# Performance work log

Hardware: AMD Instinct MI355X
Metric: run time of the kernel (lower is better)

The kernel has to match this reference:

```python
import jax, jax.numpy as jnp
import numpy as np

BS, T, SIDE, H, Z, NSPK = 2048, 34, 30, 128, 16, 1024


def _lrelu(x):
    # nn.LeakyReLU(True) -> negative_slope=1.0, i.e. identity (faithful to source)
    return x


def _gru_cell(x, h, wih, whh, bih, bhh):
    # PyTorch GRU cell, gate order (r, z, n)
    gi = x @ wih.T + bih
    gh = h @ whh.T + bhh
    ir, iz, inn = jnp.split(gi, 3, axis=-1)
    hr, hz, hn = jnp.split(gh, 3, axis=-1)
    r = jax.nn.sigmoid(ir + hr)
    z = jax.nn.sigmoid(iz + hz)
    n = jnp.tanh(inn + r * hn)
    return (1.0 - z) * n + z * h


def setup_inputs() -> dict:
    key = jax.random.key(0)
    ks = iter(jax.random.split(key, 64))
    rn = lambda shape, s=0.05: jax.random.normal(next(ks), shape, jnp.float32) * s
    inp = {}
    inp["pre_seq"] = jax.random.normal(next(ks), (BS, T, 28), jnp.float32)
    inp["beats"] = jax.random.normal(next(ks), (BS, 2, T * SIDE), jnp.float32)
    inp["in_text"] = jnp.zeros((BS, T), jnp.int32)   # unused by forward
    inp["in_audio"] = jnp.zeros((BS, 1), jnp.float32)  # unused by forward
    inp["vid_indices"] = jax.random.randint(next(ks), (BS,), 0, NSPK)
    inp["eps"] = jax.random.normal(next(ks), (BS, Z), jnp.float32)  # reparameterize noise
    # speaker embedding net
    inp["spk_table"] = rn((NSPK, Z))
    inp["spk_lin_w"] = rn((Z, Z)); inp["spk_lin_b"] = jnp.zeros((Z,))
    inp["mu_w"] = rn((Z, Z)); inp["mu_b"] = jnp.zeros((Z,))
    inp["lv_w"] = rn((Z, Z)); inp["lv_b"] = jnp.zeros((Z,))
    # per-step MLPs
    inp["squ_w"] = rn((H, 3 * SIDE)); inp["squ_b"] = jnp.zeros((H,))
    inp["oenv_w"] = rn((H, 3 * SIDE)); inp["oenv_b"] = jnp.zeros((H,))
    inp["pose_w"] = rn((16, 28)); inp["pose_b"] = jnp.zeros((16,))
    inp["out_w"] = rn((H, H + 16)); inp["out_b"] = jnp.zeros((H,))
    inp["bo_w1"] = rn((64, H)); inp["bo_b1"] = jnp.zeros((64,))
    inp["bo_w2"] = rn((27, 64)); inp["bo_b2"] = jnp.zeros((27,))
    # GRU: 4 layers, bidirectional, hidden 128; layer0 input 144, layers1-3 input 256
    inp["w_ih_l0"] = rn((2, 3 * H, H + 16)); inp["w_hh_l0"] = rn((2, 3 * H, H))
    inp["b_ih_l0"] = jnp.zeros((2, 3 * H)); inp["b_hh_l0"] = jnp.zeros((2, 3 * H))
    inp["w_ih"] = rn((3, 2, 3 * H, 2 * H)); inp["w_hh"] = rn((3, 2, 3 * H, H))
    inp["b_ih"] = jnp.zeros((3, 2, 3 * H)); inp["b_hh"] = jnp.zeros((3, 2, 3 * H))
    return inp


def reference(pre_seq, beats, in_text, in_audio, vid_indices, eps,
              spk_table, spk_lin_w, spk_lin_b, mu_w, mu_b, lv_w, lv_b,
              squ_w, squ_b, oenv_w, oenv_b, pose_w, pose_b,
              out_w, out_b, bo_w1, bo_b1, bo_w2, bo_b2,
              w_ih_l0, w_hh_l0, b_ih_l0, b_hh_l0, w_ih, w_hh, b_ih, b_hh):
    bs = beats.shape[0]
    # speaker latent
    zc0 = spk_table[vid_indices] @ spk_lin_w.T + spk_lin_b
    z_mu = zc0 @ mu_w.T + mu_b
    z_logvar = zc0 @ lv_w.T + lv_b
    z_context = z_mu + eps * jnp.exp(0.5 * z_logvar)  # reparameterize

    # sub_beats windows: pad side_size zeros on each end, window=90, stride=30
    padded = jnp.pad(beats, ((0, 0), (0, 0), (SIDE, SIDE)))
    widx = SIDE * jnp.arange(T)[:, None] + jnp.arange(3 * SIDE)[None, :]
    win = padded[:, :, widx]  # (bs, 2, T, 90)

    # batch the tiny per-step MLPs across all 34 steps at once
    squ = _lrelu(jnp.einsum('bts,os->bto', win[:, 0], squ_w) + squ_b)
    oenv = _lrelu(jnp.einsum('bts,os->bto', win[:, 1], oenv_w) + oenv_b)
    sum_out = squ + oenv                                   # (bs, T, 128)
    pose = _lrelu(jnp.einsum('bts,os->bto', pre_seq, pose_w) + pose_b)  # (bs, T, 16)
    xs = jnp.concatenate([pose, sum_out], axis=-1).transpose(1, 0, 2)   # (T, bs, 144)

    def step(h, x):
        # h: (8, bs, H) = [l0_fwd, l0_bwd, l1_fwd, ...]; seq_len==1 per step
        hs = []
        for l in range(4):
            if l == 0:
                wi, wh, bi, bh = w_ih_l0, w_hh_l0, b_ih_l0, b_hh_l0
            else:
                wi, wh, bi, bh = w_ih[l - 1], w_hh[l - 1], b_ih[l - 1], b_hh[l - 1]
            hf = _gru_cell(x, h[2 * l], wi[0], wh[0], bi[0], bh[0])
            hb = _gru_cell(x, h[2 * l + 1], wi[1], wh[1], bi[1], bh[1])
            hs += [hf, hb]
            x = jnp.concatenate([hf, hb], axis=-1)
        # output = fwd half + bwd half of top layer
        return jnp.stack(hs), hs[-2] + hs[-1]

    h0 = jnp.zeros((8, bs, H), xs.dtype)  # decoder_hidden = None -> zeros
    _, outs = jax.lax.scan(step, h0, xs)  # (T, bs, H)

    zb = jnp.broadcast_to(z_context, (T,) + z_context.shape)  # (T, bs, 16)
    feat = _lrelu(jnp.concatenate([outs, zb], axis=-1) @ out_w.T + out_b)  # (T, bs, 128)
    beat = _lrelu(feat @ bo_w1.T + bo_b1) @ bo_w2.T + bo_b2               # (T, bs, 27)
    return beat.transpose(1, 0, 2), z_context, z_mu, z_logvar
```

## Files before the change

kernel.cpp:

```cpp
#include <hip/hip_runtime.h>
#include <hip/hip_bf16.h>
#include <stdint.h>

typedef __attribute__((ext_vector_type(8))) short bfrag;
typedef __attribute__((ext_vector_type(4))) float f32x4;

__device__ __forceinline__ unsigned short f2bf(float f){
  union { float f; unsigned u; } v; v.f = f;
  unsigned r = v.u + 0x7FFFu + ((v.u >> 16) & 1u);
  return (unsigned short)(r >> 16);
}
__device__ __forceinline__ f32x4 mfma16(bfrag a, bfrag b, f32x4 c){
  return __builtin_amdgcn_mfma_f32_16x16x32_bf16(a, b, c, 0, 0, 0);
}
__device__ __forceinline__ bfrag cvt8(const float* s){
  bfrag r;
  #pragma unroll
  for (int j = 0; j < 8; ++j) r[j] = (short)f2bf(s[j]);
  return r;
}

__global__ void k_pad(const float* __restrict__ beats, unsigned short* __restrict__ pad,
                      int NG){
  int g = blockIdx.x * 256 + threadIdx.x;
  if (g >= NG) return;
  int i8 = (g % 135) * 8;
  long rc = g / 135;
  const float* src = beats + rc * 1020;
  union { unsigned short u[8]; bfrag s; } o;
  #pragma unroll
  for (int j = 0; j < 8; ++j){
    int i = i8 + j;
    float v = (i >= 30 && i < 1050) ? src[i - 30] : 0.f;
    o.u[j] = f2bf(v);
  }
  *(bfrag*)(pad + rc * 1080 + i8) = o.s;
}

__global__ void k_prep(const float* __restrict__ squ_w, const float* __restrict__ oenv_w,
                       const float* __restrict__ pose_w, const float* __restrict__ out_w,
                       const float* __restrict__ bo_w1, const float* __restrict__ bo_w2,
                       unsigned short* __restrict__ B2w, unsigned short* __restrict__ posewp,
                       unsigned short* __restrict__ B1, unsigned short* __restrict__ bow1p,
                       unsigned short* __restrict__ bow2p){
  int i = blockIdx.x * 256 + threadIdx.x;
  if (i < 24576){
    int o = i / 192, k = i - o * 192;
    float v = 0.f;
    if (k < 90) v = squ_w[o * 90 + k];
    else if (k >= 96 && k < 186) v = oenv_w[o * 90 + (k - 96)];
    B2w[i] = f2bf(v);
    return;
  }
  i -= 24576;
  if (i < 512){
    int o = i / 32, k = i - o * 32;
    posewp[i] = f2bf(k < 28 ? pose_w[o * 28 + k] : 0.f);
    return;
  }
  i -= 512;
  if (i < 36864){
    int o = i / 288, k = i - o * 288;
    float v = 0.f;
    if (k < 128) v = out_w[o * 144 + k];
    else if (k < 256) v = out_w[o * 144 + (k - 128)];
    else if (k < 272) v = out_w[o * 144 + 128 + (k - 256)];
    B1[i] = f2bf(v);
    return;
  }
  i -= 36864;
  if (i < 8192){ bow1p[i] = f2bf(bo_w1[i]); return; }
  i -= 8192;
  if (i < 2048){
    int o = i / 64, k = i - o * 64;
    bow2p[i] = f2bf(o < 27 ? bo_w2[o * 64 + k] : 0.f);
  }
}

__global__ void k_z(const int* __restrict__ vid, const float* __restrict__ eps,
                    const float* __restrict__ spk_table, const float* __restrict__ slw,
                    const float* __restrict__ slb, const float* __restrict__ muw,
                    const float* __restrict__ mub, const float* __restrict__ lvw,
                    const float* __restrict__ lvb,
                    float* __restrict__ outp, unsigned short* __restrict__ zws){
  int b = blockIdx.x * 256 + threadIdx.x;
  if (b >= 2048) return;
  const float* tr = spk_table + (long)vid[b] * 16;
  float t[16], zc0[16];
  #pragma unroll
  for (int k = 0; k < 16; ++k) t[k] = tr[k];
  #pragma unroll
  for (int j = 0; j < 16; ++j){
    float a = slb[j];
    #pragma unroll
    for (int k = 0; k < 16; ++k) a += t[k] * slw[j * 16 + k];
    zc0[j] = a;
  }
  const long ZC = 1880064, ZMU = 1912832, ZLV = 1945600;
  #pragma unroll
  for (int j = 0; j < 16; ++j){
    float mu = mub[j], lv = lvb[j];
    #pragma unroll
    for (int k = 0; k < 16; ++k){ mu += zc0[k] * muw[j * 16 + k]; lv += zc0[k] * lvw[j * 16 + k]; }
    float zc = mu + eps[b * 16 + j] * __expf(0.5f * lv);
    outp[ZMU + b * 16 + j] = mu;
    outp[ZLV + b * 16 + j] = lv;
    outp[ZC + b * 16 + j] = zc;
    zws[b * 16 + j] = f2bf(zc);
  }
}

__global__ __launch_bounds__(256) void k_x0(
    const unsigned short* __restrict__ pad, const float* __restrict__ pre_seq,
    const unsigned short* __restrict__ B2w, const unsigned short* __restrict__ posewp,
    const float* __restrict__ squ_b, const float* __restrict__ oenv_b,
    const float* __restrict__ pose_b, unsigned short* __restrict__ xbuf0){
  int bid = blockIdx.x;
  int t = bid % 34, bt = bid / 34;
  int w = threadIdx.x >> 6, lane = threadIdx.x & 63;
  int q = lane >> 4, l15 = lane & 15;
  int row = bt * 64 + w * 16 + l15;
  bfrag a[6];
  {
    const unsigned short* p0 = pad + ((long)row * 2) * 1080 + 30 * t;
    #pragma unroll
    for (int kt = 0; kt < 6; ++kt){
      int k = kt * 32 + q * 8;
      const unsigned short* src = (k < 96) ? (p0 + k) : (p0 + 1080 + (k - 96));
      const unsigned int* pu = (const unsigned int*)src;
      union { unsigned int u[4]; bfrag s; } v;
      v.u[0] = pu[0]; v.u[1] = pu[1]; v.u[2] = pu[2]; v.u[3] = pu[3];
      a[kt] = v.s;
    }
  }
  f32x4 acc[8];
  #pragma unroll
  for (int nt = 0; nt < 8; ++nt) acc[nt] = (f32x4){0.f, 0.f, 0.f, 0.f};
  #pragma unroll
  for (int kt = 0; kt < 6; ++kt)
    #pragma unroll
    for (int nt = 0; nt < 8; ++nt){
      bfrag bf = *(const bfrag*)(B2w + ((nt * 16 + l15) * 192 + kt * 32 + q * 8));
      acc[nt] = mfma16(a[kt], bf, acc[nt]);
    }
  f32x4 accp = (f32x4){0.f, 0.f, 0.f, 0.f};
  {
    float av[8];
    const float* ps = pre_seq + ((long)row * 34 + t) * 28;
    if (q < 3){
      #pragma unroll
      for (int j = 0; j < 8; ++j) av[j] = ps[q * 8 + j];
    } else {
      #pragma unroll
      for (int j = 0; j < 4; ++j){ av[j] = ps[24 + j]; av[4 + j] = 0.f; }
    }
    bfrag ap = cvt8(av);
    bfrag bp = *(const bfrag*)(posewp + (l15 * 32 + q * 8));
    accp = mfma16(ap, bp, accp);
  }
  float pb = pose_b[l15];
  int rowc = bt * 64 + w * 16 + q * 4;
  #pragma unroll
  for (int r = 0; r < 4; ++r){
    long base = ((long)(rowc + r) * 34 + t) * 160;
    xbuf0[base + l15] = f2bf(accp[r] + pb);
    xbuf0[base + 144 + l15] = 0;
  }
  #pragma unroll
  for (int nt = 0; nt < 8; ++nt){
    int c = nt * 16 + l15;
    float sb = squ_b[c] + oenv_b[c];
    #pragma unroll
    for (int r = 0; r < 4; ++r){
      long base = ((long)(rowc + r) * 34 + t) * 160;
      xbuf0[base + 16 + c] = f2bf(acc[nt][r] + sb);
    }
  }
}

template<int KIT, int KI>
__global__ __launch_bounds__(512, 2) void k_gru(
    const unsigned short* __restrict__ xin, unsigned short* __restrict__ xout,
    const float* __restrict__ wih, const float* __restrict__ whh,
    const float* __restrict__ bih, const float* __restrict__ bhh, int WK){
  __shared__ unsigned short x_lds[3][16 * (KI + 8)];
  __shared__ unsigned short h_lds[2][16 * 136];
  int d = blockIdx.x & 1, bt = blockIdx.x >> 1;
  int tid = threadIdx.x;
  int w = tid >> 6, lane = tid & 63, q = lane >> 4, l15 = lane & 15;
  const float* wihd = wih + (long)d * 384 * WK;
  const float* whhd = whh + (long)d * 384 * 128;
  int col = w * 16 + l15;
  float bi0 = bih[d * 384 + col], bi1 = bih[d * 384 + 128 + col], bi2 = bih[d * 384 + 256 + col];
  float bh0 = bhh[d * 384 + col], bh1 = bhh[d * 384 + 128 + col], bh2 = bhh[d * 384 + 256 + col];
  bfrag bgi[3][KIT];
  #pragma unroll
  for (int g = 0; g < 3; ++g)
    #pragma unroll
    for (int kt = 0; kt < KIT; ++kt){
      int k = kt * 32 + q * 8;
      if (k < WK){
        float tmp[8];
        const float* s = wihd + (long)(g * 128 + col) * WK + k;
        #pragma unroll
        for (int j = 0; j < 8; ++j) tmp[j] = s[j];
        bgi[g][kt] = cvt8(tmp);
      } else {
        bgi[g][kt] = (bfrag){0, 0, 0, 0, 0, 0, 0, 0};
      }
    }
  bfrag bwh[3][4];
  #pragma unroll
  for (int g = 0; g < 3; ++g)
    #pragma unroll
    for (int kt = 0; kt < 4; ++kt){
      float tmp[8];
      const float* s = whhd + (long)(g * 128 + col) * 128 + kt * 32 + q * 8;
      #pragma unroll
      for (int j = 0; j < 8; ++j) tmp[j] = s[j];
      bwh[g][kt] = cvt8(tmp);
    }
  const int NV = KI / 8;
  int xrow = tid / NV, xv = tid - xrow * NV;
  bool xact = (tid < 16 * NV);
  const unsigned short* xin_row = xin + ((long)(bt * 16 + (xact ? xrow : 0))) * 34 * KI;
  if (xact){
    *(bfrag*)(&x_lds[0][xrow * (KI + 8) + xv * 8]) = *(const bfrag*)(xin_row + xv * 8);
    *(bfrag*)(&x_lds[1][xrow * (KI + 8) + xv * 8]) = *(const bfrag*)(xin_row + (long)KI + xv * 8);
  }
  for (int i = tid; i < 16 * 136; i += 512) h_lds[0][i] = 0;
  __syncthreads();

  f32x4 gc0 = {0,0,0,0}, gc1 = {0,0,0,0}, gc2 = {0,0,0,0};
  #pragma unroll
  for (int kt = 0; kt < KIT; ++kt){
    bfrag xa = *(const bfrag*)(&x_lds[0][l15 * (KI + 8) + kt * 32 + q * 8]);
    gc0 = mfma16(xa, bgi[0][kt], gc0);
    gc1 = mfma16(xa, bgi[1][kt], gc1);
    gc2 = mfma16(xa, bgi[2][kt], gc2);
  }
  bfrag xpf = (bfrag){0, 0, 0, 0, 0, 0, 0, 0};
  if (xact) xpf = *(const bfrag*)(xin_row + 2L * KI + xv * 8);

  f32x4 h_old = {0,0,0,0};
  unsigned short hbf[4] = {0, 0, 0, 0};
  int rowc = bt * 16 + q * 4;
  int p = 0;
  int s1 = 1, s2 = 2;
  for (int t = 0; t < 34; ++t){
    if (t > 0){
      #pragma unroll
      for (int r = 0; r < 4; ++r)
        xout[((long)(rowc + r) * 34 + (t - 1)) * 256 + d * 128 + col] = hbf[r];
    }
    f32x4 gh0 = {0,0,0,0}, gh1 = {0,0,0,0}, gh2 = {0,0,0,0};
    #pragma unroll
    for (int kt = 0; kt < 4; ++kt){
      bfrag ha = *(const bfrag*)(&h_lds[p][l15 * 136 + kt * 32 + q * 8]);
      gh0 = mfma16(ha, bwh[0][kt], gh0);
      gh1 = mfma16(ha, bwh[1][kt], gh1);
      gh2 = mfma16(ha, bwh[2][kt], gh2);
    }
    f32x4 h_new;
    #pragma unroll
    for (int r = 0; r < 4; ++r){
      float ir = gc0[r] + bi0, iz = gc1[r] + bi1, inn = gc2[r] + bi2;
      float hr = gh0[r] + bh0, hz = gh1[r] + bh1, hn = gh2[r] + bh2;
      float rg = 1.f / (1.f + __expf(-(ir + hr)));
      float zg = 1.f / (1.f + __expf(-(iz + hz)));
      float pre = inn + rg * hn;
      float ax = fabsf(pre);
      float th = 1.f - 2.f / (__expf(2.f * ax) + 1.f);
      th = (pre < 0.f) ? -th : th;
      float hv = (1.f - zg) * th + zg * h_old[r];
      h_new[r] = hv;
      hbf[r] = f2bf(hv);
    }
    h_old = h_new;
    #pragma unroll
    for (int r = 0; r < 4; ++r)
      h_lds[1 - p][(q * 4 + r) * 136 + col] = hbf[r];
    if (t + 1 < 34){
      f32x4 gn0 = {0,0,0,0}, gn1 = {0,0,0,0}, gn2 = {0,0,0,0};
      #pragma unroll
      for (int kt = 0; kt < KIT; ++kt){
        bfrag xa = *(const bfrag*)(&x_lds[s1][l15 * (KI + 8) + kt * 32 + q * 8]);
        gn0 = mfma16(xa, bgi[0][kt], gn0);
        gn1 = mfma16(xa, bgi[1][kt], gn1);
        gn2 = mfma16(xa, bgi[2][kt], gn2);
      }
      gc0 = gn0; gc1 = gn1; gc2 = gn2;
    }
    if (xact && t + 2 < 34){
      *(bfrag*)(&x_lds[s2][xrow * (KI + 8) + xv * 8]) = xpf;
      if (t + 3 < 34) xpf = *(const bfrag*)(xin_row + (long)(t + 3) * KI + xv * 8);
    }
    s1 = (s1 == 2) ? 0 : s1 + 1;
    s2 = (s2 == 2) ? 0 : s2 + 1;
    p ^= 1;
    __syncthreads();
  }
  #pragma unroll
  for (int r = 0; r < 4; ++r)
    xout[((long)(rowc + r) * 34 + 33) * 256 + d * 128 + col] = hbf[r];
}

__global__ __launch_bounds__(512) void k_head(
    const unsigned short* __restrict__ xb, const unsigned short* __restrict__ zloc,
    const unsigned short* __restrict__ B1p, const unsigned short* __restrict__ bow1p,
    const unsigned short* __restrict__ bow2p,
    const float* __restrict__ out_b, const float* __restrict__ bo_b1,
    const float* __restrict__ bo_b2, float* __restrict__ outp){
  __shared__ unsigned short B1_lds[128 * 296];
  __shared__ unsigned short feat_lds[128 * 136];
  __shared__ unsigned short bt1_lds[128 * 72];
  int tid = threadIdx.x, w = tid >> 6, lane = tid & 63, q = lane >> 4, l15 = lane & 15;
  long rbase = (long)blockIdx.x * 128;
  for (int v = tid; v < 128 * 36; v += 512){
    int n = v / 36, kc = (v - n * 36) * 8;
    *(bfrag*)(&B1_lds[n * 296 + kc]) = *(const bfrag*)(B1p + n * 288 + kc);
  }
  __syncthreads();
  int rloc = w * 16 + l15;
  long rt = rbase + rloc;
  int bidx = (int)(rt / 34);
  bfrag a1[9];
  #pragma unroll
  for (int kt = 0; kt < 8; ++kt)
    a1[kt] = *(const bfrag*)(xb + rt * 256 + kt * 32 + q * 8);
  if (q < 2) a1[8] = *(const bfrag*)(zloc + (long)bidx * 16 + q * 8);
  else       a1[8] = (bfrag){0, 0, 0, 0, 0, 0, 0, 0};
  f32x4 acc[8];
  #pragma unroll
  for (int nt = 0; nt < 8; ++nt) acc[nt] = (f32x4){0.f, 0.f, 0.f, 0.f};
  #pragma unroll
  for (int kt = 0; kt < 9; ++kt)
    #pragma unroll
    for (int nt = 0; nt < 8; ++nt){
      bfrag b = *(const bfrag*)(&B1_lds[(nt * 16 + l15) * 296 + kt * 32 + q * 8]);
      acc[nt] = mfma16(a1[kt], b, acc[nt]);
    }
  #pragma unroll
  for (int nt = 0; nt < 8; ++nt){
    float bb = out_b[nt * 16 + l15];
    #pragma unroll
    for (int r = 0; r < 4; ++r)
      feat_lds[(w * 16 + q * 4 + r) * 136 + nt * 16 + l15] = f2bf(acc[nt][r] + bb);
  }
  __syncthreads();
  bfrag a2[4];
  #pragma unroll
  for (int kt = 0; kt < 4; ++kt)
    a2[kt] = *(const bfrag*)(&feat_lds[rloc * 136 + kt * 32 + q * 8]);
  f32x4 acc2[4];
  #pragma unroll
  for (int nt = 0; nt < 4; ++nt) acc2[nt] = (f32x4){0.f, 0.f, 0.f, 0.f};
  #pragma unroll
  for (int kt = 0; kt < 4; ++kt)
    #pragma unroll
    for (int nt = 0; nt < 4; ++nt){
      bfrag b = *(const bfrag*)(bow1p + ((nt * 16 + l15) * 128 + kt * 32 + q * 8));
      acc2[nt] = mfma16(a2[kt], b, acc2[nt]);
    }
  #pragma unroll
  for (int nt = 0; nt < 4; ++nt){
    float bb = bo_b1[nt * 16 + l15];
    #pragma unroll
    for (int r = 0; r < 4; ++r)
      bt1_lds[(w * 16 + q * 4 + r) * 72 + nt * 16 + l15] = f2bf(acc2[nt][r] + bb);
  }
  __syncthreads();
  bfrag a3[2];
  #pragma unroll
  for (int kt = 0; kt < 2; ++kt)
    a3[kt] = *(const bfrag*)(&bt1_lds[rloc * 72 + kt * 32 + q * 8]);
  f32x4 acc3[2];
  #pragma unroll
  for (int nt = 0; nt < 2; ++nt) acc3[nt] = (f32x4){0.f, 0.f, 0.f, 0.f};
  #pragma unroll
  for (int kt = 0; kt < 2; ++kt)
    #pragma unroll
    for (int nt = 0; nt < 2; ++nt){
      bfrag b = *(const bfrag*)(bow2p + ((nt * 16 + l15) * 64 + kt * 32 + q * 8));
      acc3[nt] = mfma16(a3[kt], b, acc3[nt]);
    }
  #pragma unroll
  for (int nt = 0; nt < 2; ++nt){
    int n = nt * 16 + l15;
    if (n < 27){
      float bb = bo_b2[n];
      #pragma unroll
      for (int r = 0; r < 4; ++r){
        long rowg = rbase + w * 16 + q * 4 + r;
        outp[rowg * 27 + n] = acc3[nt][r] + bb;
      }
    }
  }
}

extern "C" void kernel_launch(void* const* d_in, const int* in_sizes, int n_in,
                              void* d_out, int out_size, void* d_ws, size_t ws_size,
                              hipStream_t stream){
  (void)in_sizes; (void)n_in; (void)out_size;
  const float* pre_seq = (const float*)d_in[0];
  const float* beats   = (const float*)d_in[1];
  const int*   vid     = (const int*)d_in[4];
  const float* eps     = (const float*)d_in[5];
  const float* spk_table = (const float*)d_in[6];
  const float* slw = (const float*)d_in[7];
  const float* slb = (const float*)d_in[8];
  const float* muw = (const float*)d_in[9];
  const float* mub = (const float*)d_in[10];
  const float* lvw = (const float*)d_in[11];
  const float* lvb = (const float*)d_in[12];
  const float* squ_w = (const float*)d_in[13];
  const float* squ_b = (const float*)d_in[14];
  const float* oenv_w = (const float*)d_in[15];
  const float* oenv_b = (const float*)d_in[16];
  const float* pose_w = (const float*)d_in[17];
  const float* pose_b = (const float*)d_in[18];
  const float* out_w = (const float*)d_in[19];
  const float* out_b = (const float*)d_in[20];
  const float* bo_w1 = (const float*)d_in[21];
  const float* bo_b1 = (const float*)d_in[22];
  const float* bo_w2 = (const float*)d_in[23];
  const float* bo_b2 = (const float*)d_in[24];
  const float* w_ih_l0 = (const float*)d_in[25];
  const float* w_hh_l0 = (const float*)d_in[26];
  const float* b_ih_l0 = (const float*)d_in[27];
  const float* b_hh_l0 = (const float*)d_in[28];
  const float* w_ih = (const float*)d_in[29];
  const float* w_hh = (const float*)d_in[30];
  const float* b_ih = (const float*)d_in[31];
  const float* b_hh = (const float*)d_in[32];
  float* outp = (float*)d_out;
  unsigned short* ws = (unsigned short*)d_ws;

  const long o_z     = 0;
  const long o_B2w   = 32768;
  const long o_posew = o_B2w + 24576;
  const long o_B1    = o_posew + 512;
  const long o_bw1   = o_B1 + 36864;
  const long o_bw2   = o_bw1 + 8192;
  const long o_chunk = o_bw2 + 2048;

  int Bc;
  {
    const size_t margin = 1u << 20;
    size_t need2048 = (size_t)(o_chunk + 2048L * 25008) * 2 + margin;
    size_t need512  = (size_t)(o_chunk + 512L  * 25008) * 2 + margin;
    if      (ws_size >= need2048) Bc = 2048;
    else if (ws_size >= need512)  Bc = 512;
    else                          Bc = 128;
  }
  const int C = 2048 / Bc;
  const long o_pad = o_chunk;
  const long o_x0  = o_pad + (long)Bc * 2160;
  const long o_A   = o_x0  + (long)Bc * 5440;
  const long o_B   = o_A   + (long)Bc * 8704;

  k_prep<<<282, 256, 0, stream>>>(squ_w, oenv_w, pose_w, out_w, bo_w1, bo_w2,
                                  ws + o_B2w, ws + o_posew, ws + o_B1, ws + o_bw1, ws + o_bw2);
  k_z<<<8, 256, 0, stream>>>(vid, eps, spk_table, slw, slb, muw, mub, lvw, lvb, outp, ws + o_z);

  for (int c = 0; c < C; ++c){
    long b0 = (long)c * Bc;
    int NG = Bc * 270;
    k_pad<<<NG / 256, 256, 0, stream>>>(beats + b0 * 2040, ws + o_pad, NG);
    k_x0<<<34 * (Bc / 64), 256, 0, stream>>>(ws + o_pad, pre_seq + b0 * 952,
                                             ws + o_B2w, ws + o_posew,
                                             squ_b, oenv_b, pose_b, ws + o_x0);
    k_gru<5, 160><<<Bc / 8, 512, 0, stream>>>(ws + o_x0, ws + o_A,
                                              w_ih_l0, w_hh_l0, b_ih_l0, b_hh_l0, 144);
    k_gru<8, 256><<<Bc / 8, 512, 0, stream>>>(ws + o_A, ws + o_B,
                                              w_ih, w_hh, b_ih, b_hh, 256);
    k_gru<8, 256><<<Bc / 8, 512, 0, stream>>>(ws + o_B, ws + o_A,
                                              w_ih + 1L * 2 * 384 * 256, w_hh + 1L * 2 * 384 * 128,
                                              b_ih + 2 * 384, b_hh + 2 * 384, 256);
    k_gru<8, 256><<<Bc / 8, 512, 0, stream>>>(ws + o_A, ws + o_B,
                                              w_ih + 2L * 2 * 384 * 256, w_hh + 2L * 2 * 384 * 128,
                                              b_ih + 4 * 384, b_hh + 4 * 384, 256);
    k_head<<<Bc * 34 / 128, 512, 0, stream>>>(ws + o_B, ws + o_z,
                                              ws + o_B1, ws + o_bw1, ws + o_bw2,
                                              out_b, bo_b1, bo_b2, outp + b0 * 918);
  }
}
```

Before: 499.1 us.

## Split GRU layers into input-projection and recurrence kernels with 8-row recurrent blocks

Each fused GRU layer kernel becomes two kernels. The first computes the input-gate projections for all timesteps and stores them in bf16 in a workspace buffer. The second runs only the hidden-state recurrence, with each block handling 8 batch rows and 256 threads, so the serial chain is shorter per step and twice as many blocks run in parallel. The cost is extra global memory traffic for the gate buffer, gate inputs rounded to bf16, and half the MFMA rows wasted in the recurrence, since only 8 of the 16 are used.

```diff
diff --git a/kernel.cpp b/kernel.cpp
--- a/kernel.cpp
+++ b/kernel.cpp
@@ -3,12 +3,16 @@
 #include <stdint.h>
 
 typedef __attribute__((ext_vector_type(8))) short bfrag;
+typedef __attribute__((ext_vector_type(4))) short bf4;
 typedef __attribute__((ext_vector_type(4))) float f32x4;
 
 __device__ __forceinline__ unsigned short f2bf(float f){
   union { float f; unsigned u; } v; v.f = f;
   unsigned r = v.u + 0x7FFFu + ((v.u >> 16) & 1u);
   return (unsigned short)(r >> 16);
+}
+__device__ __forceinline__ float bf2f(unsigned short u){
+  union { unsigned u; float f; } v; v.u = ((unsigned)u) << 16; return v.f;
 }
 __device__ __forceinline__ f32x4 mfma16(bfrag a, bfrag b, f32x4 c){
   return __builtin_amdgcn_mfma_f32_16x16x32_bf16(a, b, c, 0, 0, 0);
@@ -179,20 +183,16 @@
 }
 
 template<int KIT, int KI>
-__global__ __launch_bounds__(512, 2) void k_gru(
-    const unsigned short* __restrict__ xin, unsigned short* __restrict__ xout,
-    const float* __restrict__ wih, const float* __restrict__ whh,
-    const float* __restrict__ bih, const float* __restrict__ bhh, int WK){
+__global__ __launch_bounds__(512, 2) void k_gi(
+    const unsigned short* __restrict__ xin, unsigned short* __restrict__ gi,
+    const float* __restrict__ wih, const float* __restrict__ bih, int WK){
   __shared__ unsigned short x_lds[3][16 * (KI + 8)];
-  __shared__ unsigned short h_lds[2][16 * 136];
   int d = blockIdx.x & 1, bt = blockIdx.x >> 1;
   int tid = threadIdx.x;
   int w = tid >> 6, lane = tid & 63, q = lane >> 4, l15 = lane & 15;
   const float* wihd = wih + (long)d * 384 * WK;
-  const float* whhd = whh + (long)d * 384 * 128;
   int col = w * 16 + l15;
-  float bi0 = bih[d * 384 + col], bi1 = bih[d * 384 + 128 + col], bi2 = bih[d * 384 + 256 + col];
-  float bh0 = bhh[d * 384 + col], bh1 = bhh[d * 384 + 128 + col], bh2 = bhh[d * 384 + 256 + col];
+  float bib0 = bih[d * 384 + col], bib1 = bih[d * 384 + 128 + col], bib2 = bih[d * 384 + 256 + col];
   bfrag bgi[3][KIT];
   #pragma unroll
   for (int g = 0; g < 3; ++g)
@@ -209,17 +209,6 @@
         bgi[g][kt] = (bfrag){0, 0, 0, 0, 0, 0, 0, 0};
       }
     }
-  bfrag bwh[3][4];
-  #pragma unroll
-  for (int g = 0; g < 3; ++g)
-    #pragma unroll
-    for (int kt = 0; kt < 4; ++kt){
-      float tmp[8];
-      const float* s = whhd + (long)(g * 128 + col) * 128 + kt * 32 + q * 8;
-      #pragma unroll
-      for (int j = 0; j < 8; ++j) tmp[j] = s[j];
-      bwh[g][kt] = cvt8(tmp);
-    }
   const int NV = KI / 8;
   int xrow = tid / NV, xv = tid - xrow * NV;
   bool xact = (tid < 16 * NV);
@@ -228,81 +217,134 @@
     *(bfrag*)(&x_lds[0][xrow * (KI + 8) + xv * 8]) = *(const bfrag*)(xin_row + xv * 8);
     *(bfrag*)(&x_lds[1][xrow * (KI + 8) + xv * 8]) = *(const bfrag*)(xin_row + (long)KI + xv * 8);
   }
-  for (int i = tid; i < 16 * 136; i += 512) h_lds[0][i] = 0;
   __syncthreads();
-
-  f32x4 gc0 = {0,0,0,0}, gc1 = {0,0,0,0}, gc2 = {0,0,0,0};
-  #pragma unroll
-  for (int kt = 0; kt < KIT; ++kt){
-    bfrag xa = *(const bfrag*)(&x_lds[0][l15 * (KI + 8) + kt * 32 + q * 8]);
-    gc0 = mfma16(xa, bgi[0][kt], gc0);
-    gc1 = mfma16(xa, bgi[1][kt], gc1);
-    gc2 = mfma16(xa, bgi[2][kt], gc2);
-  }
-  bfrag xpf = (bfrag){0, 0, 0, 0, 0, 0, 0, 0};
-  if (xact) xpf = *(const bfrag*)(xin_row + 2L * KI + xv * 8);
-
-  f32x4 h_old = {0,0,0,0};
-  unsigned short hbf[4] = {0, 0, 0, 0};
-  int rowc = bt * 16 + q * 4;
+  long gib = (long)(bt * 2 + d) * 34 * 3 * 2048;
+  int s0 = 0, s1 = 1, s2 = 2;
+  for (int t = 0; t < 34; ++t){
+    bfrag xpf = (bfrag){0, 0, 0, 0, 0, 0, 0, 0};
+    if (xact && t + 2 < 34)
+      xpf = *(const bfrag*)(xin_row + (long)(t + 2) * KI + xv * 8);
+    f32x4 a0 = {0,0,0,0}, a1 = {0,0,0,0}, a2 = {0,0,0,0};
+    #pragma unroll
+    for (int kt = 0; kt < KIT; ++kt){
+      bfrag xa = *(const bfrag*)(&x_lds[s0][l15 * (KI + 8) + kt * 32 + q * 8]);
+      a0 = mfma16(xa, bgi[0][kt], a0);
+      a1 = mfma16(xa, bgi[1][kt], a1);
+      a2 = mfma16(xa, bgi[2][kt], a2);
+    }
+    long tb = gib + (long)t * 3 * 2048;
+    bf4 v0, v1, v2;
+    #pragma unroll
+    for (int r = 0; r < 4; ++r){
+      v0[r] = (short)f2bf(a0[r] + bib0);
+      v1[r] = (short)f2bf(a1[r] + bib1);
+      v2[r] = (short)f2bf(a2[r] + bib2);
+    }
+    *(bf4*)(gi + tb + 0 * 2048 + col * 16 + q * 4) = v0;
+    *(bf4*)(gi + tb + 1 * 2048 + col * 16 + q * 4) = v1;
+    *(bf4*)(gi + tb + 2 * 2048 + col * 16 + q * 4) = v2;
+    if (xact && t + 2 < 34)
+      *(bfrag*)(&x_lds[s2][xrow * (KI + 8) + xv * 8]) = xpf;
+    int tmp = s0; s0 = s1; s1 = s2; s2 = tmp;
+    __syncthreads();
+  }
+}
+
+__global__ __launch_bounds__(256, 2) void k_rec(
+    const unsigned short* __restrict__ gi, unsigned short* __restrict__ xout,
+    const float* __restrict__ whh, const float* __restrict__ bhh){
+  __shared__ unsigned short h_lds[2][16 * 136];
+  int d = blockIdx.x & 1, g8 = blockIdx.x >> 1;
+  int bt16 = g8 >> 1, r16b = (g8 & 1) * 8;
+  int tid = threadIdx.x;
+  int w = tid >> 6, lane = tid & 63, q = lane >> 4, l15 = lane & 15;
+  const float* whhd = whh + (long)d * 384 * 128;
+  int c0 = w * 32 + l15, c1 = w * 32 + 16 + l15;
+  bfrag bwh[3][2][4];
+  #pragma unroll
+  for (int g = 0; g < 3; ++g)
+    #pragma unroll
+    for (int tl = 0; tl < 2; ++tl)
+      #pragma unroll
+      for (int kt = 0; kt < 4; ++kt){
+        float tmp[8];
+        const float* s = whhd + (long)(g * 128 + (tl ? c1 : c0)) * 128 + kt * 32 + q * 8;
+        #pragma unroll
+        for (int j = 0; j < 8; ++j) tmp[j] = s[j];
+        bwh[g][tl][kt] = cvt8(tmp);
+      }
+  float bh[3][2];
+  #pragma unroll
+  for (int g = 0; g < 3; ++g){
+    bh[g][0] = bhh[d * 384 + g * 128 + c0];
+    bh[g][1] = bhh[d * 384 + g * 128 + c1];
+  }
+  for (int i = tid; i < 2 * 16 * 136; i += 256) (&h_lds[0][0])[i] = 0;
+  __syncthreads();
+  int rq = (q < 2) ? q * 4 : 0;
+  long gib = (long)(bt16 * 2 + d) * 34 * 3 * 2048;
+  bf4 cur[3][2], nxt[3][2];
+  #pragma unroll
+  for (int g = 0; g < 3; ++g){
+    cur[g][0] = *(const bf4*)(gi + gib + (long)g * 2048 + c0 * 16 + r16b + rq);
+    cur[g][1] = *(const bf4*)(gi + gib + (long)g * 2048 + c1 * 16 + r16b + rq);
+  }
+  f32x4 ho[2] = {{0,0,0,0},{0,0,0,0}};
   int p = 0;
-  int s1 = 1, s2 = 2;
+  int rowc = g8 * 8 + q * 4;
   for (int t = 0; t < 34; ++t){
-    if (t > 0){
-      #pragma unroll
-      for (int r = 0; r < 4; ++r)
-        xout[((long)(rowc + r) * 34 + (t - 1)) * 256 + d * 128 + col] = hbf[r];
-    }
-    f32x4 gh0 = {0,0,0,0}, gh1 = {0,0,0,0}, gh2 = {0,0,0,0};
-    #pragma unroll
-    for (int kt = 0; kt < 4; ++kt){
-      bfrag ha = *(const bfrag*)(&h_lds[p][l15 * 136 + kt * 32 + q * 8]);
-      gh0 = mfma16(ha, bwh[0][kt], gh0);
-      gh1 = mfma16(ha, bwh[1][kt], gh1);
-      gh2 = mfma16(ha, bwh[2][kt], gh2);
-    }
-    f32x4 h_new;
-    #pragma unroll
-    for (int r = 0; r < 4; ++r){
-      float ir = gc0[r] + bi0, iz = gc1[r] + bi1, inn = gc2[r] + bi2;
-      float hr = gh0[r] + bh0, hz = gh1[r] + bh1, hn = gh2[r] + bh2;
-      float rg = 1.f / (1.f + __expf(-(ir + hr)));
-      float zg = 1.f / (1.f + __expf(-(iz + hz)));
-      float pre = inn + rg * hn;
-      float ax = fabsf(pre);
-      float th = 1.f - 2.f / (__expf(2.f * ax) + 1.f);
-      th = (pre < 0.f) ? -th : th;
-      float hv = (1.f - zg) * th + zg * h_old[r];
-      h_new[r] = hv;
-      hbf[r] = f2bf(hv);
-    }
-    h_old = h_new;
-    #pragma unroll
-    for (int r = 0; r < 4; ++r)
-      h_lds[1 - p][(q * 4 + r) * 136 + col] = hbf[r];
     if (t + 1 < 34){
-      f32x4 gn0 = {0,0,0,0}, gn1 = {0,0,0,0}, gn2 = {0,0,0,0};
-      #pragma unroll
-      for (int kt = 0; kt < KIT; ++kt){
-        bfrag xa = *(const bfrag*)(&x_lds[s1][l15 * (KI + 8) + kt * 32 + q * 8]);
-        gn0 = mfma16(xa, bgi[0][kt], gn0);
-        gn1 = mfma16(xa, bgi[1][kt], gn1);
-        gn2 = mfma16(xa, bgi[2][kt], gn2);
+      long tb = gib + (long)(t + 1) * 3 * 2048;
+      #pragma unroll
+      for (int g = 0; g < 3; ++g){
+        nxt[g][0] = *(const bf4*)(gi + tb + (long)g * 2048 + c0 * 16 + r16b + rq);
+        nxt[g][1] = *(const bf4*)(gi + tb + (long)g * 2048 + c1 * 16 + r16b + rq);
       }
-      gc0 = gn0; gc1 = gn1; gc2 = gn2;
-    }
-    if (xact && t + 2 < 34){
-      *(bfrag*)(&x_lds[s2][xrow * (KI + 8) + xv * 8]) = xpf;
-      if (t + 3 < 34) xpf = *(const bfrag*)(xin_row + (long)(t + 3) * KI + xv * 8);
-    }
-    s1 = (s1 == 2) ? 0 : s1 + 1;
-    s2 = (s2 == 2) ? 0 : s2 + 1;
+    }
+    bfrag ha[4];
+    #pragma unroll
+    for (int kt = 0; kt < 4; ++kt)
+      ha[kt] = *(const bfrag*)(&h_lds[p][l15 * 136 + kt * 32 + q * 8]);
+    f32x4 gh[3][2];
+    #pragma unroll
+    for (int g = 0; g < 3; ++g){ gh[g][0] = (f32x4){0,0,0,0}; gh[g][1] = (f32x4){0,0,0,0}; }
+    #pragma unroll
+    for (int kt = 0; kt < 4; ++kt)
+      #pragma unroll
+      for (int g = 0; g < 3; ++g){
+        gh[g][0] = mfma16(ha[kt], bwh[g][0][kt], gh[g][0]);
+        gh[g][1] = mfma16(ha[kt], bwh[g][1][kt], gh[g][1]);
+      }
+    #pragma unroll
+    for (int tl = 0; tl < 2; ++tl){
+      int cc = tl ? c1 : c0;
+      #pragma unroll
+      for (int r = 0; r < 4; ++r){
+        float ir  = bf2f((unsigned short)cur[0][tl][r]);
+        float iz  = bf2f((unsigned short)cur[1][tl][r]);
+        float inn = bf2f((unsigned short)cur[2][tl][r]);
+        float hr = gh[0][tl][r] + bh[0][tl];
+        float hz = gh[1][tl][r] + bh[1][tl];
+        float hn = gh[2][tl][r] + bh[2][tl];
+        float rg = 1.f / (1.f + __expf(-(ir + hr)));
+        float zg = 1.f / (1.f + __expf(-(iz + hz)));
+        float pre = inn + rg * hn;
+        float ax = fabsf(pre);
+        float th = 1.f - 2.f / (__expf(2.f * ax) + 1.f);
+        th = (pre < 0.f) ? -th : th;
+        float hv = (1.f - zg) * th + zg * ho[tl][r];
+        ho[tl][r] = hv;
+        unsigned short hb = f2bf(hv);
+        h_lds[1 - p][(q * 4 + r) * 136 + cc] = hb;
+        if (q < 2)
+          xout[((long)(rowc + r) * 34 + t) * 256 + d * 128 + cc] = hb;
+      }
+    }
+    #pragma unroll
+    for (int g = 0; g < 3; ++g){ cur[g][0] = nxt[g][0]; cur[g][1] = nxt[g][1]; }
     p ^= 1;
     __syncthreads();
   }
-  #pragma unroll
-  for (int r = 0; r < 4; ++r)
-    xout[((long)(rowc + r) * 34 + 33) * 256 + d * 128 + col] = hbf[r];
 }
 
 __global__ __launch_bounds__(512) void k_head(
@@ -444,12 +486,15 @@
   const long o_bw2   = o_bw1 + 8192;
   const long o_chunk = o_bw2 + 2048;
 
+  const long PERROW = 51120;
   int Bc;
   {
     const size_t margin = 1u << 20;
-    size_t need2048 = (size_t)(o_chunk + 2048L * 25008) * 2 + margin;
-    size_t need512  = (size_t)(o_chunk + 512L  * 25008) * 2 + margin;
+    size_t need2048 = (size_t)(o_chunk + 2048L * PERROW) * 2 + margin;
+    size_t need1024 = (size_t)(o_chunk + 1024L * PERROW) * 2 + margin;
+    size_t need512  = (size_t)(o_chunk + 512L  * PERROW) * 2 + margin;
     if      (ws_size >= need2048) Bc = 2048;
+    else if (ws_size >= need1024) Bc = 1024;
     else if (ws_size >= need512)  Bc = 512;
     else                          Bc = 128;
   }
@@ -458,6 +503,7 @@
   const long o_x0  = o_pad + (long)Bc * 2160;
   const long o_A   = o_x0  + (long)Bc * 5440;
   const long o_B   = o_A   + (long)Bc * 8704;
+  const long o_GI  = o_B   + (long)Bc * 8704;
 
   k_prep<<<282, 256, 0, stream>>>(squ_w, oenv_w, pose_w, out_w, bo_w1, bo_w2,
                                   ws + o_B2w, ws + o_posew, ws + o_B1, ws + o_bw1, ws + o_bw2);
@@ -470,16 +516,18 @@
     k_x0<<<34 * (Bc / 64), 256, 0, stream>>>(ws + o_pad, pre_seq + b0 * 952,
                                              ws + o_B2w, ws + o_posew,
                                              squ_b, oenv_b, pose_b, ws + o_x0);
-    k_gru<5, 160><<<Bc / 8, 512, 0, stream>>>(ws + o_x0, ws + o_A,
-                                              w_ih_l0, w_hh_l0, b_ih_l0, b_hh_l0, 144);
-    k_gru<8, 256><<<Bc / 8, 512, 0, stream>>>(ws + o_A, ws + o_B,
-                                              w_ih, w_hh, b_ih, b_hh, 256);
-    k_gru<8, 256><<<Bc / 8, 512, 0, stream>>>(ws + o_B, ws + o_A,
-                                              w_ih + 1L * 2 * 384 * 256, w_hh + 1L * 2 * 384 * 128,
-                                              b_ih + 2 * 384, b_hh + 2 * 384, 256);
-    k_gru<8, 256><<<Bc / 8, 512, 0, stream>>>(ws + o_A, ws + o_B,
-                                              w_ih + 2L * 2 * 384 * 256, w_hh + 2L * 2 * 384 * 128,
-                                              b_ih + 4 * 384, b_hh + 4 * 384, 256);
+    k_gi<5, 160><<<Bc / 8, 512, 0, stream>>>(ws + o_x0, ws + o_GI, w_ih_l0, b_ih_l0, 144);
+    k_rec<<<Bc / 4, 256, 0, stream>>>(ws + o_GI, ws + o_A, w_hh_l0, b_hh_l0);
+    k_gi<8, 256><<<Bc / 8, 512, 0, stream>>>(ws + o_A, ws + o_GI, w_ih, b_ih, 256);
+    k_rec<<<Bc / 4, 256, 0, stream>>>(ws + o_GI, ws + o_B, w_hh, b_hh);
+    k_gi<8, 256><<<Bc / 8, 512, 0, stream>>>(ws + o_B, ws + o_GI,
+                                             w_ih + 1L * 2 * 384 * 256, b_ih + 2 * 384, 256);
+    k_rec<<<Bc / 4, 256, 0, stream>>>(ws + o_GI, ws + o_A,
+                                      w_hh + 1L * 2 * 384 * 128, b_hh + 2 * 384);
+    k_gi<8, 256><<<Bc / 8, 512, 0, stream>>>(ws + o_A, ws + o_GI,
+                                             w_ih + 2L * 2 * 384 * 256, b_ih + 4 * 384, 256);
+    k_rec<<<Bc / 4, 256, 0, stream>>>(ws + o_GI, ws + o_B,
+                                      w_hh + 2L * 2 * 384 * 128, b_hh + 4 * 384);
     k_head<<<Bc * 34 / 128, 512, 0, stream>>>(ws + o_B, ws + o_z,
                                               ws + o_B1, ws + o_bw1, ws + o_bw2,
                                               out_b, bo_b1, bo_b2, outp + b0 * 918);
```

Result: slower. 763.7 us (+53.0%).
